# Kernel tuning notes

Hardware: AMD Instinct MI355X
Metric: run time of the kernel (lower is better)

Reference implementation:

```python
import jax, jax.numpy as jnp
import numpy as np

N = 4096          # total atoms
N_MOL = 32        # molecules in the batch
BOX = 20.0        # box edge (Angstrom)
CUTOFF = 5.0      # cutoff_upper
MAX_PAIRS = 32768 # max_num_pairs
# loop=False -> only i<j pairs, no self interactions


def setup_inputs() -> dict:
    key = jax.random.key(0)
    k1, k2 = jax.random.split(key)
    pos = jax.random.uniform(k1, (N, 3), dtype=jnp.float32) * BOX
    batch = jnp.sort(jax.random.randint(k2, (N,), 0, N_MOL)).astype(jnp.int32)
    return {"pos": pos, "batch": batch}


def _neighbor_pairs(pos, batch):
    n = pos.shape[0]
    # static upper-triangle candidate pairs (loop=False excludes the diagonal)
    ii_np, jj_np = np.triu_indices(n, k=1)
    ii = jnp.asarray(ii_np, jnp.int32)
    jj = jnp.asarray(jj_np, jnp.int32)

    vec = pos[ii] - pos[jj]                         # [P,3]
    dist = jnp.sqrt(jnp.sum(vec * vec, axis=-1))    # [P]
    mask = (batch[ii] == batch[jj]) & (dist < CUTOFF)

    # compaction: valid pairs get consecutive slots, invalid ones are dropped
    slot = jnp.where(mask, jnp.cumsum(mask) - 1, MAX_PAIRS)

    neighbors = jnp.full((2, MAX_PAIRS), -1, jnp.int32)
    neighbors = neighbors.at[0, slot].set(ii, mode="drop")
    neighbors = neighbors.at[1, slot].set(jj, mode="drop")
    distances = jnp.zeros((MAX_PAIRS,), pos.dtype).at[slot].set(dist, mode="drop")
    distance_vecs = jnp.zeros((MAX_PAIRS, 3), pos.dtype).at[slot].set(vec, mode="drop")
    return neighbors, distances, distance_vecs


def reference(pos, batch):
    # matches DistanceCellList.forward return order: (neighbors, distances, distance_vecs)
    neighbors, distances, distance_vecs = _neighbor_pairs(pos, batch)
    return neighbors, distances, distance_vecs
```

## Files before the change

### kernel.cpp

```cpp
#include <hip/hip_runtime.h>

#define NATOMS 4096
#define MAXP   32768
#define CUTOFF 5.0f
#define NBLK   512
#define TPB    512
#define WPB    8
#define PSTRIDE 64
#define WRITER  (NBLK - 1)
#define POLLN   30000
#define FLAGMAGIC 0xC0FFEE11u

typedef unsigned long long u64;

__device__ __forceinline__ unsigned ctag(int q) { return 0xFACE0000u ^ (unsigned)q; }
__device__ __forceinline__ unsigned ptag(int q) { return 0x5EED7A00u ^ (unsigned)q; }

__device__ int count_rows_scalar(const float* __restrict__ pos,
                                 const int* __restrict__ batch, int r0) {
#pragma clang fp contract(off)
    int c = 0;
    for (int i = r0; i < r0 + WPB; ++i) {
        const int b = batch[i];
        const float xi = pos[3*i], yi = pos[3*i+1], zi = pos[3*i+2];
        for (int j = i + 1; j < NATOMS; ++j) {
            if (batch[j] != b) break;
            float vx = xi - pos[3*j], vy = yi - pos[3*j+1], vz = zi - pos[3*j+2];
            float d2 = vx*vx + vy*vy + vz*vz;
            if (sqrtf(d2) < CUTOFF) ++c;
        }
    }
    return c;
}

__global__ __launch_bounds__(TPB)
void fused_k(const float* __restrict__ pos,
             const int*   __restrict__ batch,
             u64*         __restrict__ bsumD,
             u64*         __restrict__ prefx,
             u64*         __restrict__ flagp,
             float*       __restrict__ out) {
#pragma clang fp contract(off)
    const int tid  = threadIdx.x;
    const int p    = blockIdx.x;
    const int w    = tid >> 6;
    const int lane = tid & 63;
    const int i    = p * WPB + w;

    const int b = batch[i];
    const float xi = pos[3*i], yi = pos[3*i+1], zi = pos[3*i+2];

    __shared__ float spair[WPB][PSTRIDE * 5];
    float* rowp = &spair[w][0];

    int c = 0;
    for (int j0 = i + 1; j0 < NATOMS; j0 += 128) {
        const int jA = j0 + lane;
        const int jB = jA + 64;
        const bool inA = jA < NATOMS;
        const bool inB = jB < NATOMS;
        int bA = -1, bB = -1;
        float axp = 0.f, ayp = 0.f, azp = 0.f;
        float bxp = 0.f, byp = 0.f, bzp = 0.f;
        if (inA) { bA = batch[jA]; axp = pos[3*jA]; ayp = pos[3*jA+1]; azp = pos[3*jA+2]; }
        if (inB) { bB = batch[jB]; bxp = pos[3*jB]; byp = pos[3*jB+1]; bzp = pos[3*jB+2]; }
        {
            float vx = xi - axp, vy = yi - ayp, vz = zi - azp;
            float d2 = vx*vx + vy*vy + vz*vz;
            float d  = sqrtf(d2);
            bool valid = inA && (bA == b) && (d < CUTOFF);
            u64 m = __ballot(valid);
            if (valid) {
                int r = c + __popcll(m & ((1ULL << lane) - 1ULL));
                if (r < PSTRIDE) {
                    float* q = rowp + r * 5;
                    q[0] = (float)jA; q[1] = d; q[2] = vx; q[3] = vy; q[4] = vz;
                }
            }
            c += __popcll(m);
        }
        {
            float vx = xi - bxp, vy = yi - byp, vz = zi - bzp;
            float d2 = vx*vx + vy*vy + vz*vz;
            float d  = sqrtf(d2);
            bool valid = inB && (bB == b) && (d < CUTOFF);
            u64 m = __ballot(valid);
            if (valid) {
                int r = c + __popcll(m & ((1ULL << lane) - 1ULL));
                if (r < PSTRIDE) {
                    float* q = rowp + r * 5;
                    q[0] = (float)jB; q[1] = d; q[2] = vx; q[3] = vy; q[4] = vz;
                }
            }
            c += __popcll(m);
        }
        if (__any((inA && (bA != b)) || (inB && (bB != b)))) break;
    }

    __shared__ int ls[WPB];
    __shared__ int wsum[WPB];
    __shared__ u64 lacc[WPB];
    __shared__ u64 sfp, spp;

    if (lane == 0) ls[w] = c;
    __syncthreads();

    if (tid == 0) {
        int bs = 0;
        for (int r = 0; r < WPB; ++r) bs += ls[r];
        __hip_atomic_store(&bsumD[p], ((u64)ctag(p) << 32) | (unsigned)bs,
                           __ATOMIC_RELAXED, __HIP_MEMORY_SCOPE_AGENT);
    }

    int total, mypfx;

    if (p == WRITER) {
        const int q = tid;
        u64 t = __hip_atomic_load(&bsumD[q], __ATOMIC_RELAXED, __HIP_MEMORY_SCOPE_AGENT);
        for (int it = 0; (unsigned)(t >> 32) != ctag(q) && it < POLLN; ++it)
            t = __hip_atomic_load(&bsumD[q], __ATOMIC_RELAXED, __HIP_MEMORY_SCOPE_AGENT);
        int val = ((unsigned)(t >> 32) == ctag(q)) ? (int)(t & 0xFFFFFFFFu)
                                                   : count_rows_scalar(pos, batch, q * WPB);
        int inc = val;
        for (int o = 1; o < 64; o <<= 1) { int v = __shfl_up(inc, o); if (lane >= o) inc += v; }
        if (lane == 63) wsum[w] = inc;
        __syncthreads();
        int woff = 0;
        for (int r = 0; r < w; ++r) woff += wsum[r];
        int excl = woff + inc - val;
        __hip_atomic_store(&prefx[q], ((u64)ptag(q) << 32) | (unsigned)excl,
                           __ATOMIC_RELAXED, __HIP_MEMORY_SCOPE_AGENT);
        int tt = 0;
        for (int r = 0; r < WPB; ++r) tt += wsum[r];
        total = tt;
        __syncthreads();
        if (tid == 0)
            __hip_atomic_store(flagp, ((u64)FLAGMAGIC << 32) | (unsigned)total,
                               __ATOMIC_RELAXED, __HIP_MEMORY_SCOPE_AGENT);
        int own = 0;
        for (int r = 0; r < WPB; ++r) own += ls[r];
        mypfx = total - own;
    } else {
        if (tid == 0) {
            u64 f  = __hip_atomic_load(flagp, __ATOMIC_RELAXED, __HIP_MEMORY_SCOPE_AGENT);
            u64 pe = __hip_atomic_load(&prefx[p], __ATOMIC_RELAXED, __HIP_MEMORY_SCOPE_AGENT);
            for (int it = 0;
                 ((unsigned)(f >> 32) != FLAGMAGIC || (unsigned)(pe >> 32) != ptag(p)) && it < POLLN;
                 ++it) {
                f  = __hip_atomic_load(flagp, __ATOMIC_RELAXED, __HIP_MEMORY_SCOPE_AGENT);
                pe = __hip_atomic_load(&prefx[p], __ATOMIC_RELAXED, __HIP_MEMORY_SCOPE_AGENT);
            }
            sfp = f; spp = pe;
        }
        __syncthreads();
        const u64 f = sfp, pe = spp;
        if ((unsigned)(f >> 32) == FLAGMAGIC && (unsigned)(pe >> 32) == ptag(p)) {
            total = (int)(f & 0xFFFFFFFFu);
            mypfx = (int)(pe & 0xFFFFFFFFu);
        } else {
            const int q = tid;
            u64 t = __hip_atomic_load(&bsumD[q], __ATOMIC_RELAXED, __HIP_MEMORY_SCOPE_AGENT);
            for (int it = 0; (unsigned)(t >> 32) != ctag(q) && it < POLLN; ++it)
                t = __hip_atomic_load(&bsumD[q], __ATOMIC_RELAXED, __HIP_MEMORY_SCOPE_AGENT);
            int a = ((unsigned)(t >> 32) == ctag(q)) ? (int)(t & 0xFFFFFFFFu)
                                                     : count_rows_scalar(pos, batch, q * WPB);
            u64 acc = ((u64)(unsigned)a << 32) | (unsigned)(q < p ? a : 0);
            for (int o = 32; o; o >>= 1) acc += __shfl_down(acc, o);
            if (lane == 0) lacc[w] = acc;
            __syncthreads();
            u64 g = 0;
            for (int r = 0; r < WPB; ++r) g += lacc[r];
            total = (int)(g >> 32);
            mypfx = (int)(g & 0xFFFFFFFFu);
        }
    }

    int rowbase = mypfx;
    for (int r = 0; r < w; ++r) rowbase += ls[r];

    {
        int t = total + p * TPB + tid;
        if (t < MAXP) {
            out[t]          = -1.0f;
            out[MAXP + t]   = -1.0f;
            out[2*MAXP + t] =  0.0f;
            float* vv = out + 3*MAXP + 3*t;
            vv[0] = 0.f; vv[1] = 0.f; vv[2] = 0.f;
        }
    }

    if (c <= PSTRIDE) {
        if (lane < c) {
            int slot = rowbase + lane;
            if (slot < MAXP) {
                const float* q = rowp + lane * 5;
                out[slot]          = (float)i;
                out[MAXP + slot]   = q[0];
                out[2*MAXP + slot] = q[1];
                float* vv = out + 3*MAXP + 3*slot;
                vv[0] = q[2]; vv[1] = q[3]; vv[2] = q[4];
            }
        }
    } else {
        int slotbase = rowbase;
        for (int j0 = i + 1; j0 < NATOMS; j0 += 64) {
            int j = j0 + lane;
            bool in = j < NATOMS;
            int bj = in ? batch[j] : -1;
            bool same = in && (bj == b);
            float vx = 0.f, vy = 0.f, vz = 0.f, d = 0.f;
            bool valid = false;
            if (same) {
                vx = xi - pos[3*j]; vy = yi - pos[3*j+1]; vz = zi - pos[3*j+2];
                float d2 = vx*vx + vy*vy + vz*vz;
                d = sqrtf(d2);
                valid = d < CUTOFF;
            }
            u64 m = __ballot(valid);
            if (valid) {
                int slot = slotbase + __popcll(m & ((1ULL << lane) - 1ULL));
                if (slot < MAXP) {
                    out[slot]          = (float)i;
                    out[MAXP + slot]   = (float)j;
                    out[2*MAXP + slot] = d;
                    float* vv = out + 3*MAXP + 3*slot;
                    vv[0] = vx; vv[1] = vy; vv[2] = vz;
                }
            }
            slotbase += __popcll(m);
            if (__any(in && (bj != b))) break;
        }
    }
}

extern "C" void kernel_launch(void* const* d_in, const int* in_sizes, int n_in,
                              void* d_out, int out_size, void* d_ws, size_t ws_size,
                              hipStream_t stream) {
    const float* pos   = (const float*)d_in[0];
    const int*   batch = (const int*)d_in[1];
    float* out = (float*)d_out;

    u64* wsu   = (u64*)d_ws;
    u64* bsumD = wsu;
    u64* prefx = wsu + NBLK;
    u64* flagp = wsu + 2 * NBLK;

    fused_k<<<NBLK, TPB, 0, stream>>>(pos, batch, bsumD, prefx, flagp, out);
}
```

Baseline: 9.934 us.

## Replace single-writer prefix broadcast with per-block decentralized scan of block counts

```diff
diff --git a/kernel.cpp b/kernel.cpp
--- a/kernel.cpp
+++ b/kernel.cpp
@@ -7,14 +7,11 @@
 #define TPB    512
 #define WPB    8
 #define PSTRIDE 64
-#define WRITER  (NBLK - 1)
-#define POLLN   30000
-#define FLAGMAGIC 0xC0FFEE11u
+#define POLLN   4000
 
 typedef unsigned long long u64;
 
 __device__ __forceinline__ unsigned ctag(int q) { return 0xFACE0000u ^ (unsigned)q; }
-__device__ __forceinline__ unsigned ptag(int q) { return 0x5EED7A00u ^ (unsigned)q; }
 
 __device__ int count_rows_scalar(const float* __restrict__ pos,
                                  const int* __restrict__ batch, int r0) {
@@ -37,8 +34,6 @@
 void fused_k(const float* __restrict__ pos,
              const int*   __restrict__ batch,
              u64*         __restrict__ bsumD,
-             u64*         __restrict__ prefx,
-             u64*         __restrict__ flagp,
              float*       __restrict__ out) {
 #pragma clang fp contract(off)
     const int tid  = threadIdx.x;
@@ -98,9 +93,7 @@
     }
 
     __shared__ int ls[WPB];
-    __shared__ int wsum[WPB];
     __shared__ u64 lacc[WPB];
-    __shared__ u64 sfp, spp;
 
     if (lane == 0) ls[w] = c;
     __syncthreads();
@@ -112,79 +105,31 @@
                            __ATOMIC_RELAXED, __HIP_MEMORY_SCOPE_AGENT);
     }
 
-    int total, mypfx;
-
-    if (p == WRITER) {
-        const int q = tid;
-        u64 t = __hip_atomic_load(&bsumD[q], __ATOMIC_RELAXED, __HIP_MEMORY_SCOPE_AGENT);
-        for (int it = 0; (unsigned)(t >> 32) != ctag(q) && it < POLLN; ++it)
-            t = __hip_atomic_load(&bsumD[q], __ATOMIC_RELAXED, __HIP_MEMORY_SCOPE_AGENT);
-        int val = ((unsigned)(t >> 32) == ctag(q)) ? (int)(t & 0xFFFFFFFFu)
-                                                   : count_rows_scalar(pos, batch, q * WPB);
-        int inc = val;
-        for (int o = 1; o < 64; o <<= 1) { int v = __shfl_up(inc, o); if (lane >= o) inc += v; }
-        if (lane == 63) wsum[w] = inc;
-        __syncthreads();
-        int woff = 0;
-        for (int r = 0; r < w; ++r) woff += wsum[r];
-        int excl = woff + inc - val;
-        __hip_atomic_store(&prefx[q], ((u64)ptag(q) << 32) | (unsigned)excl,
-                           __ATOMIC_RELAXED, __HIP_MEMORY_SCOPE_AGENT);
-        int tt = 0;
-        for (int r = 0; r < WPB; ++r) tt += wsum[r];
-        total = tt;
-        __syncthreads();
-        if (tid == 0)
-            __hip_atomic_store(flagp, ((u64)FLAGMAGIC << 32) | (unsigned)total,
-                               __ATOMIC_RELAXED, __HIP_MEMORY_SCOPE_AGENT);
-        int own = 0;
-        for (int r = 0; r < WPB; ++r) own += ls[r];
-        mypfx = total - own;
-    } else {
-        if (tid == 0) {
-            u64 f  = __hip_atomic_load(flagp, __ATOMIC_RELAXED, __HIP_MEMORY_SCOPE_AGENT);
-            u64 pe = __hip_atomic_load(&prefx[p], __ATOMIC_RELAXED, __HIP_MEMORY_SCOPE_AGENT);
-            for (int it = 0;
-                 ((unsigned)(f >> 32) != FLAGMAGIC || (unsigned)(pe >> 32) != ptag(p)) && it < POLLN;
-                 ++it) {
-                f  = __hip_atomic_load(flagp, __ATOMIC_RELAXED, __HIP_MEMORY_SCOPE_AGENT);
-                pe = __hip_atomic_load(&prefx[p], __ATOMIC_RELAXED, __HIP_MEMORY_SCOPE_AGENT);
-            }
-            sfp = f; spp = pe;
-        }
-        __syncthreads();
-        const u64 f = sfp, pe = spp;
-        if ((unsigned)(f >> 32) == FLAGMAGIC && (unsigned)(pe >> 32) == ptag(p)) {
-            total = (int)(f & 0xFFFFFFFFu);
-            mypfx = (int)(pe & 0xFFFFFFFFu);
-        } else {
-            const int q = tid;
-            u64 t = __hip_atomic_load(&bsumD[q], __ATOMIC_RELAXED, __HIP_MEMORY_SCOPE_AGENT);
-            for (int it = 0; (unsigned)(t >> 32) != ctag(q) && it < POLLN; ++it)
-                t = __hip_atomic_load(&bsumD[q], __ATOMIC_RELAXED, __HIP_MEMORY_SCOPE_AGENT);
-            int a = ((unsigned)(t >> 32) == ctag(q)) ? (int)(t & 0xFFFFFFFFu)
-                                                     : count_rows_scalar(pos, batch, q * WPB);
-            u64 acc = ((u64)(unsigned)a << 32) | (unsigned)(q < p ? a : 0);
-            for (int o = 32; o; o >>= 1) acc += __shfl_down(acc, o);
-            if (lane == 0) lacc[w] = acc;
-            __syncthreads();
-            u64 g = 0;
-            for (int r = 0; r < WPB; ++r) g += lacc[r];
-            total = (int)(g >> 32);
-            mypfx = (int)(g & 0xFFFFFFFFu);
-        }
-    }
+    const int q = tid;
+    u64 t = __hip_atomic_load(&bsumD[q], __ATOMIC_RELAXED, __HIP_MEMORY_SCOPE_AGENT);
+    for (int it = 0; (unsigned)(t >> 32) != ctag(q) && it < POLLN; ++it)
+        t = __hip_atomic_load(&bsumD[q], __ATOMIC_RELAXED, __HIP_MEMORY_SCOPE_AGENT);
+    int a = ((unsigned)(t >> 32) == ctag(q)) ? (int)(t & 0xFFFFFFFFu)
+                                             : count_rows_scalar(pos, batch, q * WPB);
+    u64 acc = ((u64)(unsigned)a << 32) | (unsigned)(q < p ? a : 0);
+    for (int o = 32; o; o >>= 1) acc += __shfl_down(acc, o);
+    if (lane == 0) lacc[w] = acc;
+    __syncthreads();
+    u64 g = 0;
+    for (int r = 0; r < WPB; ++r) g += lacc[r];
+    const int total = (int)(g >> 32);
+    const int mypfx = (int)(g & 0xFFFFFFFFu);
 
     int rowbase = mypfx;
     for (int r = 0; r < w; ++r) rowbase += ls[r];
 
     {
-        int t = total + p * TPB + tid;
-        if (t < MAXP) {
-            out[t]          = -1.0f;
-            out[MAXP + t]   = -1.0f;
-            out[2*MAXP + t] =  0.0f;
-            float* vv = out + 3*MAXP + 3*t;
+        int t2 = total + p * TPB + tid;
+        if (t2 < MAXP) {
+            out[t2]          = -1.0f;
+            out[MAXP + t2]   = -1.0f;
+            out[2*MAXP + t2] =  0.0f;
+            float* vv = out + 3*MAXP + 3*t2;
             vv[0] = 0.f; vv[1] = 0.f; vv[2] = 0.f;
         }
     }
@@ -193,12 +138,12 @@
         if (lane < c) {
             int slot = rowbase + lane;
             if (slot < MAXP) {
-                const float* q = rowp + lane * 5;
+                const float* qq = rowp + lane * 5;
                 out[slot]          = (float)i;
-                out[MAXP + slot]   = q[0];
-                out[2*MAXP + slot] = q[1];
+                out[MAXP + slot]   = qq[0];
+                out[2*MAXP + slot] = qq[1];
                 float* vv = out + 3*MAXP + 3*slot;
-                vv[0] = q[2]; vv[1] = q[3]; vv[2] = q[4];
+                vv[0] = qq[2]; vv[1] = qq[3]; vv[2] = qq[4];
             }
         }
     } else {
@@ -238,12 +183,8 @@
                               hipStream_t stream) {
     const float* pos   = (const float*)d_in[0];
     const int*   batch = (const int*)d_in[1];
-    float* out = (float*)d_out;
+    float* out   = (float*)d_out;
+    u64*   bsumD = (u64*)d_ws;
 
-    u64* wsu   = (u64*)d_ws;
-    u64* bsumD = wsu;
-    u64* prefx = wsu + NBLK;
-    u64* flagp = wsu + 2 * NBLK;
-
-    fused_k<<<NBLK, TPB, 0, stream>>>(pos, batch, bsumD, prefx, flagp, out);
+    fused_k<<<NBLK, TPB, 0, stream>>>(pos, batch, bsumD, out);
 }
```

New measurement: 11.78 us. 18.6% more time.
